# Optimization experiments

Hardware: AMD Instinct MI355X
Metric: run time of the kernel (lower is better)

The kernel has to match this reference:

```python
import jax, jax.numpy as jnp
import numpy as np

B, M, D, DE = 2, 256, 256, 64  # batch, tokens, in_dim, dep_embed_dim


def setup_inputs() -> dict:
    key = jax.random.key(0)
    ks = jax.random.split(key, 10)
    features = jax.random.normal(ks[0], (B, M + 1, D), jnp.float32)
    dep_type_adj = jax.random.normal(ks[1], (B, M, M, DE), jnp.float32)
    adj = (jax.random.uniform(ks[2], (B, M, M)) < 0.05).astype(jnp.int32)
    idx = jnp.arange(M)
    adj = adj.at[:, idx, idx].set(1)
    asp_start = jax.random.randint(ks[3], (B,), 0, 200, dtype=jnp.int32)
    asp_end = asp_start + 16
    s = lambda fan_in: 1.0 / np.sqrt(fan_in)
    Wz = jax.random.normal(ks[4], (D, D), jnp.float32) * s(D)
    bz = jax.random.normal(ks[5], (D,), jnp.float32) * s(D)
    Wa = jax.random.normal(ks[6], (D + DE + D,), jnp.float32) * s(D + DE + D)
    Wm = jax.random.normal(ks[7], (D, D + DE), jnp.float32) * s(D + DE)
    Wh = jax.random.normal(ks[8], (D, 2 * D), jnp.float32) * s(2 * D)
    return dict(features=features, dep_type_adj=dep_type_adj, deprel_adj=adj,
                asp_start=asp_start, asp_end=asp_end,
                Wz=Wz, bz=bz, Wa=Wa, Wm=Wm, Wh=Wh)


def reference(features, dep_type_adj, deprel_adj, asp_start, asp_end, Wz, bz, Wa, Wm, Wh):
    # z_linear
    zf = features @ Wz.T + bz                              # [B, M+1, D]
    f = zf[:, 1:]                                          # token feats [B, M, D]
    asp = zf[0, 1:]                                        # NOTE: original indexes features[0] (batch 0)

    # candidate neighbors for node i: out-edges (i,j) then in-edges (j,i) -> 2M slots
    dep_cat = jnp.concatenate([dep_type_adj, jnp.swapaxes(dep_type_adj, 1, 2)], axis=2)  # [B,M,2M,DE]
    mask = jnp.concatenate([deprel_adj, jnp.swapaxes(deprel_adj, 1, 2)], axis=2) != 0    # [B,M,2M]

    # attention_layer weight split over [dep | neighbor_feat | aspect_feat]
    wa_dep, wa_nf, wa_asp = Wa[:DE], Wa[DE:DE + D], Wa[DE + D:]
    s = (jnp.einsum('bike,e->bik', dep_cat, wa_dep)
         + jnp.tile(f @ wa_nf, (1, 2))[:, None, :]
         + (asp @ wa_asp)[None, :, None])                  # [B,M,2M]
    s = jnp.where(s > 0, s, 0.01 * s)                      # LeakyReLU(0.01)
    big_neg = jnp.finfo(s.dtype).min
    w = jax.nn.softmax(jnp.where(mask, s, big_neg), axis=-1)
    w = jnp.where(mask, w, 0.0)                            # edge-softmax over valid neighbors

    # w_m over [dep | neighbor_feat]
    Wm_dep, Wm_f = Wm[:, :DE], Wm[:, DE:]
    nf_proj = jnp.tile(f @ Wm_f.T, (1, 2, 1))              # [B,2M,D], neighbor part (i-independent)
    msg = jax.nn.relu(jnp.einsum('bike,de->bikd', dep_cat, Wm_dep) + nf_proj[:, None])  # [B,M,2M,D]
    fused = jnp.einsum('bik,bikd->bid', w, msg)            # weighted aggregate [B,M,D]

    # w_h over [fused | aspect]
    out_asp = jax.nn.relu(fused @ Wh[:, :D].T + (asp @ Wh[:, D:].T)[None])  # [B,M,D]

    # only aspect-span nodes are updated; +1 offset into the token axis
    pos = jnp.arange(M)
    upd = (pos[None, :] >= asp_start[:, None]) & (pos[None, :] < asp_end[:, None])  # [B,M]
    tokens = jnp.where(upd[..., None], out_asp, features[:, 1:])
    return jnp.concatenate([features[:, :1], tokens], axis=1)  # dropout is identity at inference
```

## Files before the change

kernel.cpp:

```cpp
#include <hip/hip_runtime.h>
#include <hip/hip_bf16.h>
#include <cstdint>

#define BB 2
#define MM 256
#define DD 256
#define DE 64
#define K2 (2*MM)
#define WM_LD (DD+DE)
#define WH_LD (2*DD)

__device__ float g_fz    [MM*DD];
__device__ float g_fproj [BB*MM*DD];
__device__ float g_fnf   [BB*MM];
__device__ float g_WzT   [DD*DD];
__device__ float g_WmT   [DD*DD];
__device__ float g_WmDepT[DE*DD];
__device__ float g_WhT   [2*DD*DD];

__global__ __launch_bounds__(256) void k_tr(const float* __restrict__ Wz,
                                            const float* __restrict__ Wm,
                                            const float* __restrict__ Wh,
                                            const float4* __restrict__ src,
                                            float4* __restrict__ dst, int n4) {
  const int t = threadIdx.x;
  const int blk = blockIdx.x;
  if (blk < 256) {
    const int d = blk;
    g_WzT[t*DD + d] = Wz[(size_t)d*DD + t];
  } else if (blk < 512) {
    const int d = blk - 256;
    g_WmT[t*DD + d] = Wm[(size_t)d*WM_LD + DE + t];
    if (t < DE) g_WmDepT[t*DD + d] = Wm[(size_t)d*WM_LD + t];
  } else {
    const int idx = blk - 512;
    const int d = idx & 255, half = idx >> 8;
    g_WhT[(size_t)(half*DD + t)*DD + d] = Wh[(size_t)d*WH_LD + half*DD + t];
  }
  const int gidx = blk*256 + t;
  if (gidx < n4) dst[gidx] = src[gidx];
}

__global__ __launch_bounds__(256) void k_pre(const float* __restrict__ feats,
                                             const float* __restrict__ bz,
                                             const float* __restrict__ Wa) {
  const int blk = blockIdx.x;
  const int b   = blk >> 7;
  const int m0  = (blk & 127) * 2;
  const int t   = threadIdx.x;

  __shared__ float fin[2][DD];
  __shared__ float fzsh[2][DD];

  fin[0][t] = feats[((size_t)b*(MM+1) + m0 + 1)*DD + t];
  fin[1][t] = feats[((size_t)b*(MM+1) + m0 + 2)*DD + t];
  __syncthreads();

  float a0 = 0.f, a1 = 0.f;
  #pragma unroll 8
  for (int e4 = 0; e4 < DD/4; ++e4) {
    const float4 f0 = *(const float4*)&fin[0][e4*4];
    const float4 f1 = *(const float4*)&fin[1][e4*4];
    const float w0 = g_WzT[(e4*4+0)*DD + t];
    const float w1 = g_WzT[(e4*4+1)*DD + t];
    const float w2 = g_WzT[(e4*4+2)*DD + t];
    const float w3 = g_WzT[(e4*4+3)*DD + t];
    a0 += f0.x*w0 + f0.y*w1 + f0.z*w2 + f0.w*w3;
    a1 += f1.x*w0 + f1.y*w1 + f1.z*w2 + f1.w*w3;
  }
  const float bzt = bz[t];
  a0 += bzt; a1 += bzt;
  fzsh[0][t] = a0; fzsh[1][t] = a1;
  if (b == 0) {
    g_fz[(size_t)(m0    )*DD + t] = a0;
    g_fz[(size_t)(m0 + 1)*DD + t] = a1;
  }
  __syncthreads();

  const int wv = t >> 6, lane = t & 63;
  if (wv < 2) {
    float p = 0.f;
    for (int e = lane; e < DD; e += 64) p += fzsh[wv][e] * Wa[DE + e];
    for (int off = 32; off > 0; off >>= 1) p += __shfl_down(p, off, 64);
    if (lane == 0) g_fnf[b*MM + m0 + wv] = p;
  }

  float p0 = 0.f, p1 = 0.f;
  #pragma unroll 8
  for (int e4 = 0; e4 < DD/4; ++e4) {
    const float4 f0 = *(const float4*)&fzsh[0][e4*4];
    const float4 f1 = *(const float4*)&fzsh[1][e4*4];
    const float w0 = g_WmT[(e4*4+0)*DD + t];
    const float w1 = g_WmT[(e4*4+1)*DD + t];
    const float w2 = g_WmT[(e4*4+2)*DD + t];
    const float w3 = g_WmT[(e4*4+3)*DD + t];
    p0 += f0.x*w0 + f0.y*w1 + f0.z*w2 + f0.w*w3;
    p1 += f1.x*w0 + f1.y*w1 + f1.z*w2 + f1.w*w3;
  }
  g_fproj[((size_t)b*MM + m0    )*DD + t] = p0;
  g_fproj[((size_t)b*MM + m0 + 1)*DD + t] = p1;
}

__global__ __launch_bounds__(256) void k_attn(const float* __restrict__ dta,
                                              const int*   __restrict__ adj,
                                              const int*   __restrict__ a_start,
                                              const int*   __restrict__ a_end,
                                              const float* __restrict__ Wa,
                                              float* __restrict__ out) {
  const int b = blockIdx.x >> 4;
  const int r = blockIdx.x & 15;
  const int i = a_start[b] + r;
  if (i >= a_end[b] || i >= MM) return;
  const int t = threadIdx.x;
  const int lane = t & 63, wv = t >> 6;

  __shared__ int   act[K2];
  __shared__ float sv [K2];
  __shared__ int   wcnt[8];
  __shared__ float wr  [4];
  __shared__ float wrm [4];
  __shared__ float wrs [4];
  __shared__ float wadep[DE];
  __shared__ float fz0[DD];
  __shared__ float depsh[64*DE];
  __shared__ float fused_sh[DD];

  const int mval0 = adj[((size_t)b*MM + i)*MM + t];
  const int mval1 = adj[((size_t)b*MM + t)*MM + i];
  const float myfz = g_fz[(size_t)i*DD + t];
  fz0[t] = myfz;
  if (t < DE) wadep[t] = Wa[t];

  {
    float p = myfz * Wa[DE + DD + t];
    for (int off = 32; off > 0; off >>= 1) p += __shfl_down(p, off, 64);
    if (lane == 0) wr[wv] = p;
  }

  const bool on0 = (mval0 != 0);
  const bool on1 = (mval1 != 0);
  const unsigned long long b0 = __ballot(on0);
  const unsigned long long b1 = __ballot(on1);
  if (lane == 0) { wcnt[wv] = __popcll(b0); wcnt[4+wv] = __popcll(b1); }
  __syncthreads();
  const float aspdot_i = wr[0] + wr[1] + wr[2] + wr[3];
  const int tot0 = wcnt[0] + wcnt[1] + wcnt[2] + wcnt[3];
  const int na   = tot0 + wcnt[4] + wcnt[5] + wcnt[6] + wcnt[7];
  {
    int off0 = 0, off1 = tot0;
    for (int w2 = 0; w2 < wv; ++w2) { off0 += wcnt[w2]; off1 += wcnt[4+w2]; }
    off0 += __popcll(b0 & ((1ull << lane) - 1ull));
    off1 += __popcll(b1 & ((1ull << lane) - 1ull));
    if (on0) act[off0] = t;
    if (on1) act[off1] = MM + t;
  }
  __syncthreads();

  for (int j = t; j < na; j += 256) {
    const int k = act[j];
    const float* dv = (k < MM) ? dta + (((size_t)b*MM + i)*MM + k)*DE
                               : dta + (((size_t)b*MM + (k - MM))*MM + i)*DE;
    float s = 0.f;
    const float4* dv4 = (const float4*)dv;
    #pragma unroll
    for (int e4 = 0; e4 < DE/4; ++e4) {
      const float4 v = dv4[e4];
      s += v.x*wadep[4*e4] + v.y*wadep[4*e4+1] + v.z*wadep[4*e4+2] + v.w*wadep[4*e4+3];
    }
    s += g_fnf[b*MM + (k & (MM-1))] + aspdot_i;
    sv[j] = (s > 0.f) ? s : 0.01f * s;
  }
  {
    float part = -3.4e38f;
    for (int j = t; j < na; j += 256) part = fmaxf(part, sv[j]);
    for (int off = 32; off > 0; off >>= 1) part = fmaxf(part, __shfl_down(part, off, 64));
    if (lane == 0) wrm[wv] = part;
  }
  __syncthreads();
  const float mx = fmaxf(fmaxf(wrm[0], wrm[1]), fmaxf(wrm[2], wrm[3]));
  {
    float psum = 0.f;
    for (int j = t; j < na; j += 256) { float e = expf(sv[j] - mx); sv[j] = e; psum += e; }
    for (int off = 32; off > 0; off >>= 1) psum += __shfl_down(psum, off, 64);
    if (lane == 0) wrs[wv] = psum;
  }
  __syncthreads();
  const float inv = 1.f / (wrs[0] + wrs[1] + wrs[2] + wrs[3]);

  const int d = t;
  float wm[DE];
  #pragma unroll 8
  for (int e = 0; e < DE; ++e) wm[e] = g_WmDepT[e*DD + d];
  float acc = 0.f;
  for (int base = 0; base < na; base += 64) {
    const int cnt = min(64, na - base);
    const int nf4 = cnt * (DE/4);
    for (int q = t; q < nf4; q += 256) {
      const int jl = q >> 4, e4 = q & 15;
      const int k = act[base + jl];
      const float* dv = (k < MM) ? dta + (((size_t)b*MM + i)*MM + k)*DE
                                 : dta + (((size_t)b*MM + (k - MM))*MM + i)*DE;
      ((float4*)(depsh + jl*DE))[e4] = ((const float4*)dv)[e4];
    }
    __syncthreads();
    for (int jl = 0; jl < cnt; ++jl) {
      const float* dp = depsh + jl*DE;
      float dot = 0.f;
      #pragma unroll
      for (int e4 = 0; e4 < DE/4; ++e4) {
        const float4 v = *(const float4*)(dp + 4*e4);
        dot += v.x*wm[4*e4] + v.y*wm[4*e4+1] + v.z*wm[4*e4+2] + v.w*wm[4*e4+3];
      }
      const int k = act[base + jl];
      float msg = dot + g_fproj[((size_t)b*MM + (k & (MM-1)))*DD + d];
      msg = (msg > 0.f) ? msg : 0.f;
      acc += sv[base + jl] * msg;
    }
    __syncthreads();
  }
  fused_sh[d] = acc * inv;
  __syncthreads();

  float o = 0.f;
  #pragma unroll 8
  for (int e = 0; e < DD; ++e) o += fused_sh[e] * g_WhT[(size_t)e*DD + d];
  #pragma unroll 8
  for (int e = 0; e < DD; ++e) o += fz0[e] * g_WhT[(size_t)(DD + e)*DD + d];
  out[((size_t)b*(MM+1) + i + 1)*DD + d] = (o > 0.f) ? o : 0.f;
}

extern "C" void kernel_launch(void* const* d_in, const int* in_sizes, int n_in,
                              void* d_out, int out_size, void* d_ws, size_t ws_size,
                              hipStream_t stream) {
  const float* feats   = (const float*)d_in[0];
  const float* dta     = (const float*)d_in[1];
  const int*   adj     = (const int*)  d_in[2];
  const int*   a_start = (const int*)  d_in[3];
  const int*   a_end   = (const int*)  d_in[4];
  const float* Wz      = (const float*)d_in[5];
  const float* bz      = (const float*)d_in[6];
  const float* Wa      = (const float*)d_in[7];
  const float* Wm      = (const float*)d_in[8];
  const float* Wh      = (const float*)d_in[9];
  float* out = (float*)d_out;

  const int n4 = BB*(MM+1)*DD/4;
  k_tr  <<<1024, 256, 0, stream>>>(Wz, Wm, Wh, (const float4*)feats, (float4*)out, n4);
  k_pre <<<BB*MM/2, 256, 0, stream>>>(feats, bz, Wa);
  k_attn<<<BB*16, 256, 0, stream>>>(dta, adj, a_start, a_end, Wa, out);
}
```

Before: 155.3 us.

## Precompute aspect projections upstream and reuse first dep tile in attention kernel

Moves the aspect dot product and the aspect half of the Wh projection into the earlier z-linear kernel, so k_attn no longer computes them per row. The score pass now uses four lanes per edge and keeps the first 64 edge embeddings in padded shared memory, where the message pass reuses them instead of reloading. It also caches fnf in shared memory, applies the softmax normalisation to the weights directly, loads the Wm weights early, and sets launch bounds to one block per SM. In exchange the first kernel does more work for batch 0, and the larger register use may lower occupancy.

```diff
diff --git a/kernel.cpp b/kernel.cpp
--- a/kernel.cpp
+++ b/kernel.cpp
@@ -9,10 +9,13 @@
 #define K2 (2*MM)
 #define WM_LD (DD+DE)
 #define WH_LD (2*DD)
+#define DEP_LD 68
 
 __device__ float g_fz    [MM*DD];
 __device__ float g_fproj [BB*MM*DD];
 __device__ float g_fnf   [BB*MM];
+__device__ float g_aspdot[MM];
+__device__ float g_asph  [MM*DD];
 __device__ float g_WzT   [DD*DD];
 __device__ float g_WmT   [DD*DD];
 __device__ float g_WmDepT[DE*DD];
@@ -83,6 +86,12 @@
     for (int e = lane; e < DD; e += 64) p += fzsh[wv][e] * Wa[DE + e];
     for (int off = 32; off > 0; off >>= 1) p += __shfl_down(p, off, 64);
     if (lane == 0) g_fnf[b*MM + m0 + wv] = p;
+  } else if (b == 0) {
+    const int rr = wv - 2;
+    float p = 0.f;
+    for (int e = lane; e < DD; e += 64) p += fzsh[rr][e] * Wa[DE + DD + e];
+    for (int off = 32; off > 0; off >>= 1) p += __shfl_down(p, off, 64);
+    if (lane == 0) g_aspdot[m0 + rr] = p;
   }
 
   float p0 = 0.f, p1 = 0.f;
@@ -99,43 +108,58 @@
   }
   g_fproj[((size_t)b*MM + m0    )*DD + t] = p0;
   g_fproj[((size_t)b*MM + m0 + 1)*DD + t] = p1;
-}
-
-__global__ __launch_bounds__(256) void k_attn(const float* __restrict__ dta,
-                                              const int*   __restrict__ adj,
-                                              const int*   __restrict__ a_start,
-                                              const int*   __restrict__ a_end,
-                                              const float* __restrict__ Wa,
-                                              float* __restrict__ out) {
+
+  if (b == 0) {
+    float q0 = 0.f, q1 = 0.f;
+    #pragma unroll 8
+    for (int e4 = 0; e4 < DD/4; ++e4) {
+      const float4 f0 = *(const float4*)&fzsh[0][e4*4];
+      const float4 f1 = *(const float4*)&fzsh[1][e4*4];
+      const float w0 = g_WhT[(size_t)(DD + e4*4+0)*DD + t];
+      const float w1 = g_WhT[(size_t)(DD + e4*4+1)*DD + t];
+      const float w2 = g_WhT[(size_t)(DD + e4*4+2)*DD + t];
+      const float w3 = g_WhT[(size_t)(DD + e4*4+3)*DD + t];
+      q0 += f0.x*w0 + f0.y*w1 + f0.z*w2 + f0.w*w3;
+      q1 += f1.x*w0 + f1.y*w1 + f1.z*w2 + f1.w*w3;
+    }
+    g_asph[(size_t)(m0    )*DD + t] = q0;
+    g_asph[(size_t)(m0 + 1)*DD + t] = q1;
+  }
+}
+
+__global__ __launch_bounds__(256, 1) void k_attn(const float* __restrict__ dta,
+                                                 const int*   __restrict__ adj,
+                                                 const int*   __restrict__ a_start,
+                                                 const int*   __restrict__ a_end,
+                                                 const float* __restrict__ Wa,
+                                                 float* __restrict__ out) {
   const int b = blockIdx.x >> 4;
   const int r = blockIdx.x & 15;
   const int i = a_start[b] + r;
   if (i >= a_end[b] || i >= MM) return;
   const int t = threadIdx.x;
   const int lane = t & 63, wv = t >> 6;
+  const int d = t;
 
   __shared__ int   act[K2];
   __shared__ float sv [K2];
   __shared__ int   wcnt[8];
-  __shared__ float wr  [4];
   __shared__ float wrm [4];
   __shared__ float wrs [4];
   __shared__ float wadep[DE];
-  __shared__ float fz0[DD];
-  __shared__ float depsh[64*DE];
+  __shared__ float fnfsh[MM];
+  __shared__ float depsh[64*DEP_LD];
   __shared__ float fused_sh[DD];
 
   const int mval0 = adj[((size_t)b*MM + i)*MM + t];
   const int mval1 = adj[((size_t)b*MM + t)*MM + i];
-  const float myfz = g_fz[(size_t)i*DD + t];
-  fz0[t] = myfz;
+  float wm[DE];
+  #pragma unroll
+  for (int e = 0; e < DE; ++e) wm[e] = g_WmDepT[e*DD + d];
+  fnfsh[t] = g_fnf[b*MM + t];
   if (t < DE) wadep[t] = Wa[t];
-
-  {
-    float p = myfz * Wa[DE + DD + t];
-    for (int off = 32; off > 0; off >>= 1) p += __shfl_down(p, off, 64);
-    if (lane == 0) wr[wv] = p;
-  }
+  const float aspdot_i = g_aspdot[i];
+  const float asph_i   = g_asph[(size_t)i*DD + d];
 
   const bool on0 = (mval0 != 0);
   const bool on1 = (mval1 != 0);
@@ -143,7 +167,6 @@
   const unsigned long long b1 = __ballot(on1);
   if (lane == 0) { wcnt[wv] = __popcll(b0); wcnt[4+wv] = __popcll(b1); }
   __syncthreads();
-  const float aspdot_i = wr[0] + wr[1] + wr[2] + wr[3];
   const int tot0 = wcnt[0] + wcnt[1] + wcnt[2] + wcnt[3];
   const int na   = tot0 + wcnt[4] + wcnt[5] + wcnt[6] + wcnt[7];
   {
@@ -156,20 +179,35 @@
   }
   __syncthreads();
 
-  for (int j = t; j < na; j += 256) {
-    const int k = act[j];
-    const float* dv = (k < MM) ? dta + (((size_t)b*MM + i)*MM + k)*DE
-                               : dta + (((size_t)b*MM + (k - MM))*MM + i)*DE;
-    float s = 0.f;
-    const float4* dv4 = (const float4*)dv;
-    #pragma unroll
-    for (int e4 = 0; e4 < DE/4; ++e4) {
-      const float4 v = dv4[e4];
-      s += v.x*wadep[4*e4] + v.y*wadep[4*e4+1] + v.z*wadep[4*e4+2] + v.w*wadep[4*e4+3];
-    }
-    s += g_fnf[b*MM + (k & (MM-1))] + aspdot_i;
-    sv[j] = (s > 0.f) ? s : 0.01f * s;
-  }
+  const int jj = t >> 2, sub = t & 3;
+  for (int base = 0; base < na; base += 64) {
+    const int j = base + jj;
+    float p = 0.f; int k = 0;
+    if (j < na) {
+      k = act[j];
+      const float* dv = (k < MM) ? dta + (((size_t)b*MM + i)*MM + k)*DE
+                                 : dta + (((size_t)b*MM + (k - MM))*MM + i)*DE;
+      const float4* dv4 = (const float4*)dv + sub*4;
+      const float4 v0 = dv4[0], v1 = dv4[1], v2 = dv4[2], v3 = dv4[3];
+      const float* wa = wadep + sub*16;
+      p = v0.x*wa[0]  + v0.y*wa[1]  + v0.z*wa[2]  + v0.w*wa[3]
+        + v1.x*wa[4]  + v1.y*wa[5]  + v1.z*wa[6]  + v1.w*wa[7]
+        + v2.x*wa[8]  + v2.y*wa[9]  + v2.z*wa[10] + v2.w*wa[11]
+        + v3.x*wa[12] + v3.y*wa[13] + v3.z*wa[14] + v3.w*wa[15];
+      if (base == 0) {
+        float4* ds = (float4*)(depsh + jj*DEP_LD + sub*16);
+        ds[0] = v0; ds[1] = v1; ds[2] = v2; ds[3] = v3;
+      }
+    }
+    p += __shfl_xor(p, 1, 64);
+    p += __shfl_xor(p, 2, 64);
+    if (j < na && sub == 0) {
+      const float s = p + fnfsh[k & (MM-1)] + aspdot_i;
+      sv[j] = (s > 0.f) ? s : 0.01f * s;
+    }
+  }
+  __syncthreads();
+
   {
     float part = -3.4e38f;
     for (int j = t; j < na; j += 256) part = fmaxf(part, sv[j]);
@@ -186,46 +224,52 @@
   }
   __syncthreads();
   const float inv = 1.f / (wrs[0] + wrs[1] + wrs[2] + wrs[3]);
-
-  const int d = t;
-  float wm[DE];
-  #pragma unroll 8
-  for (int e = 0; e < DE; ++e) wm[e] = g_WmDepT[e*DD + d];
+  for (int j = t; j < na; j += 256) sv[j] *= inv;
+  __syncthreads();
+
   float acc = 0.f;
   for (int base = 0; base < na; base += 64) {
     const int cnt = min(64, na - base);
-    const int nf4 = cnt * (DE/4);
-    for (int q = t; q < nf4; q += 256) {
-      const int jl = q >> 4, e4 = q & 15;
+    if (base > 0) {
+      __syncthreads();
+      const int nf4 = cnt * (DE/4);
+      for (int q = t; q < nf4; q += 256) {
+        const int jl = q >> 4, e4 = q & 15;
+        const int k = act[base + jl];
+        const float* dv = (k < MM) ? dta + (((size_t)b*MM + i)*MM + k)*DE
+                                   : dta + (((size_t)b*MM + (k - MM))*MM + i)*DE;
+        *(float4*)(depsh + jl*DEP_LD + e4*4) = ((const float4*)dv)[e4];
+      }
+      __syncthreads();
+    }
+    #pragma unroll 2
+    for (int jl = 0; jl < cnt; ++jl) {
       const int k = act[base + jl];
-      const float* dv = (k < MM) ? dta + (((size_t)b*MM + i)*MM + k)*DE
-                                 : dta + (((size_t)b*MM + (k - MM))*MM + i)*DE;
-      ((float4*)(depsh + jl*DE))[e4] = ((const float4*)dv)[e4];
-    }
-    __syncthreads();
-    for (int jl = 0; jl < cnt; ++jl) {
-      const float* dp = depsh + jl*DE;
+      const float* dp = depsh + jl*DEP_LD;
       float dot = 0.f;
       #pragma unroll
       for (int e4 = 0; e4 < DE/4; ++e4) {
         const float4 v = *(const float4*)(dp + 4*e4);
         dot += v.x*wm[4*e4] + v.y*wm[4*e4+1] + v.z*wm[4*e4+2] + v.w*wm[4*e4+3];
       }
-      const int k = act[base + jl];
       float msg = dot + g_fproj[((size_t)b*MM + (k & (MM-1)))*DD + d];
       msg = (msg > 0.f) ? msg : 0.f;
       acc += sv[base + jl] * msg;
     }
-    __syncthreads();
-  }
-  fused_sh[d] = acc * inv;
-  __syncthreads();
-
-  float o = 0.f;
+  }
+  fused_sh[d] = acc;
+  __syncthreads();
+
+  float o = asph_i;
   #pragma unroll 8
-  for (int e = 0; e < DD; ++e) o += fused_sh[e] * g_WhT[(size_t)e*DD + d];
-  #pragma unroll 8
-  for (int e = 0; e < DD; ++e) o += fz0[e] * g_WhT[(size_t)(DD + e)*DD + d];
+  for (int e4 = 0; e4 < DD/4; ++e4) {
+    const float f0 = fused_sh[4*e4+0], f1 = fused_sh[4*e4+1];
+    const float f2 = fused_sh[4*e4+2], f3 = fused_sh[4*e4+3];
+    o += f0 * g_WhT[(size_t)(4*e4+0)*DD + d]
+       + f1 * g_WhT[(size_t)(4*e4+1)*DD + d]
+       + f2 * g_WhT[(size_t)(4*e4+2)*DD + d]
+       + f3 * g_WhT[(size_t)(4*e4+3)*DD + d];
+  }
   out[((size_t)b*(MM+1) + i + 1)*DD + d] = (o > 0.f) ? o : 0.f;
 }
 
```

After: 147.9 us. -4.8%, faster.
